# Kernel optimization log

Hardware: AMD Instinct MI355X
Metric: run time of the kernel (lower is better)

The kernel has to match this reference:

```python
import jax, jax.numpy as jnp
import numpy as np

BITS_I, BITS_W = 8, 8
GROUP = 36
DIR_I = (0, 1, 2, 3)
DIR_W = (0, 1, 2, 3)


def bfp_quantize(x, bits, group_size, perm):
    """Block floating point: groups of `group_size` elements (after permuting
    axes by `perm` and flattening) share one exponent (exponent of max abs);
    mantissas are rounded to `bits` signed bits."""
    inv_perm = tuple(np.argsort(perm))
    xp = jnp.transpose(x, perm)
    shape = xp.shape
    flat = xp.reshape(-1)
    n = flat.shape[0]
    pad = (-n) % group_size
    flat = jnp.pad(flat, (0, pad))
    g = flat.reshape(-1, group_size)
    maxabs = jnp.max(jnp.abs(g), axis=1, keepdims=True)
    e = jnp.floor(jnp.log2(jnp.maximum(maxabs, jnp.float32(1e-38))))
    scale = jnp.exp2(e - (bits - 1))  # shared group exponent, `bits` mantissa bits
    qmax = 2 ** (bits - 1) - 1
    q = jnp.clip(jnp.round(g / scale), -qmax - 1, qmax) * scale
    q = jnp.where(maxabs == 0, jnp.float32(0), q)
    out = q.reshape(-1)[:n].reshape(shape)
    return jnp.transpose(out, inv_perm)


def conv2d(x, w, b, stride=1, padding=1, dilation=1, groups=1):
    out = jax.lax.conv_general_dilated(
        x, w,
        window_strides=(stride, stride),
        padding=[(padding, padding), (padding, padding)],
        rhs_dilation=(dilation, dilation),
        feature_group_count=groups,
        dimension_numbers=('NCHW', 'OIHW', 'NCHW'))
    if b is not None:
        out = out + b[None, :, None, None]
    return out


def setup_inputs() -> dict:
    key = jax.random.key(0)
    k1, k2, k3 = jax.random.split(key, 3)
    x = jax.random.normal(k1, (16, 256, 56, 56), dtype=jnp.float32)
    fan_in = 256 * 3 * 3
    bound = 1.0 / np.sqrt(fan_in)
    weight = jax.random.uniform(k2, (256, 256, 3, 3), dtype=jnp.float32,
                                minval=-np.sqrt(6.0 / fan_in), maxval=np.sqrt(6.0 / fan_in))
    bias = jax.random.uniform(k3, (256,), dtype=jnp.float32, minval=-bound, maxval=bound)
    return {"x": x, "weight": weight, "bias": bias}


def reference(x, weight, bias):
    xq = bfp_quantize(x, BITS_I, GROUP, DIR_I)
    wq = bfp_quantize(weight, BITS_W, GROUP, DIR_W)
    return conv2d(xq, wq, bias, stride=1, padding=1, dilation=1, groups=1)
```

## Files before the change

kernel.cpp:

```cpp
#include <hip/hip_runtime.h>

typedef short short8 __attribute__((ext_vector_type(8)));
typedef float f32x4 __attribute__((ext_vector_type(4)));
typedef unsigned short u16;
typedef __attribute__((address_space(3))) unsigned lds_u32_t;
typedef __attribute__((address_space(1))) const unsigned glb_u32_t;

namespace {
constexpr int NIMG = 16;
constexpr int CIN  = 256;
constexpr int HIMG = 56;
constexpr int WIMG = 56;
constexpr int KOUT = 256;
constexpr int PIX  = HIMG * WIMG;
constexpr int HPAD = 58;
constexpr int PP   = HPAD * HPAD;
constexpr int TILES = 26;
constexpr int NX   = NIMG * CIN * PIX;
constexpr int NWEL = KOUT * CIN * 9;
constexpr int XQ_HALVES = NIMG * 32 * PP * 8;
constexpr int CHUNK = 8 * PIX;
constexpr int XBLK = NIMG * 32;
constexpr int WB   = 64;
constexpr int NWG  = NIMG * TILES * 4;
constexpr int CPX  = NWG / 8;
}

__global__ __launch_bounds__(256) void quant_fused(
        const float* __restrict__ x, u16* __restrict__ xq2,
        const float* __restrict__ wsrc, u16* __restrict__ wt3) {
    __shared__ u16 ot[CHUNK];
    const int b = blockIdx.x;
    const int t = threadIdx.x;

    if (b < XBLK) {
        const long s  = (long)b * CHUNK;
        const int  g0 = (int)(s / 36);
        const int  g1 = (int)((s + CHUNK - 1) / 36);

        if (t < 228) {
            int ph, pw;
            if (t < 58)       { ph = 0;  pw = t; }
            else if (t < 116) { ph = 57; pw = t - 58; }
            else { int r = t - 116; ph = 1 + (r >> 1); pw = (r & 1) * 57; }
            *(uint4*)(xq2 + ((size_t)b * PP + ph * HPAD + pw) * 8) =
                make_uint4(0, 0, 0, 0);
        }

        for (int g = g0 + t; g <= g1; g += 256) {
            const long e0 = (long)g * 36;
            float v[36];
            if (e0 + 36 <= (long)NX) {
                const float4* p4 = (const float4*)(x + e0);
#pragma unroll
                for (int j = 0; j < 9; j++) {
                    float4 q4 = p4[j];
                    v[4*j+0] = q4.x; v[4*j+1] = q4.y;
                    v[4*j+2] = q4.z; v[4*j+3] = q4.w;
                }
            } else {
                for (int j = 0; j < 36; j++)
                    v[j] = (e0 + j < (long)NX) ? x[e0 + j] : 0.f;
            }
            float ma = 0.f;
#pragma unroll
            for (int j = 0; j < 36; j++) ma = fmaxf(ma, fabsf(v[j]));
            float scale = 0.f, rinv = 0.f;
            if (ma != 0.f) {
                float e = floorf(log2f(ma));
                scale = exp2f(e - 7.f);
                rinv  = exp2f(7.f - e);
            }
            const long o = e0 - s;
#pragma unroll
            for (int j = 0; j < 36; j += 2) {
                float qa = fminf(fmaxf(rintf(v[j]   * rinv), -128.f), 127.f) * scale;
                float qb = fminf(fmaxf(rintf(v[j+1] * rinv), -128.f), 127.f) * scale;
                uint pk = (__float_as_uint(qa) >> 16)
                        | ((__float_as_uint(qb) >> 16) << 16);
                long oo = o + j;
                if (oo >= 0 && oo < CHUNK)
                    *(uint*)&ot[oo] = pk;
            }
        }
        __syncthreads();

        for (int p = t; p < PIX; p += 256) {
            short8 o8;
#pragma unroll
            for (int cl = 0; cl < 8; cl++)
                o8[cl] = (short)ot[cl * PIX + p];
            int ph = p / WIMG + 1, pw = p % WIMG + 1;
            *(short8*)(xq2 + ((size_t)b * PP + ph * HPAD + pw) * 8) = o8;
        }
    } else {
        int g = (b - XBLK) * 256 + t;
        int base = g * 36;
        float v[36];
        const float4* p4 = (const float4*)(wsrc + base);
#pragma unroll
        for (int j = 0; j < 9; j++) {
            float4 tt = p4[j];
            v[4*j+0] = tt.x; v[4*j+1] = tt.y; v[4*j+2] = tt.z; v[4*j+3] = tt.w;
        }
        float ma = 0.f;
#pragma unroll
        for (int j = 0; j < 36; j++) ma = fmaxf(ma, fabsf(v[j]));
        float scale = 0.f, rinv = 0.f;
        if (ma != 0.f) {
            float e = floorf(log2f(ma));
            scale = exp2f(e - 7.f);
            rinv  = exp2f(7.f - e);
        }
        int k  = g >> 6;
        int c0 = (g & 63) * 4;
#pragma unroll
        for (int j = 0; j < 36; j++) {
            float q = rintf(v[j] * rinv);
            q = fminf(fmaxf(q, -128.f), 127.f) * scale;
            int c  = c0 + j / 9;
            int rs = j % 9;
            int idx = ((((rs * 4 + (c >> 6)) * 8 + ((c >> 3) & 7)) * KOUT) + k) * 8 + (c & 7);
            wt3[idx] = (u16)(__float_as_uint(q) >> 16);
        }
    }
}

#define LOADA(dst_, c_)                                                        \
    {                                                                          \
        const int csp_ = (c_) / 18;                                            \
        const int rsk_ = ((c_) % 18) / 2;                                      \
        const int sub_ = (c_) & 1;                                             \
        const u16* ap_ = wt3 + (rsk_ * 4 + csp_) * 16384 + sub_ * 8192;        \
        _Pragma("unroll")                                                      \
        for (int i_ = 0; i_ < 4; i_++)                                         \
            dst_[i_] = *(const short8*)(ap_ + aOff + i_ * 128);                \
    }

__global__ __launch_bounds__(256, 4) void conv_kernel(
        const u16* __restrict__ xq2, const u16* __restrict__ wt3,
        const float* __restrict__ bias, float* __restrict__ out) {
    __shared__ u16 lB[16384];

    const int tid  = threadIdx.x;
    const int lane = tid & 63;
    const int wv   = tid >> 6;

    const int work = ((int)blockIdx.x & 7) * CPX + ((int)blockIdx.x >> 3);
    const int kq   = work & 3;
    const int pair = work >> 2;
    const int n    = pair / TILES;
    const int t0   = (pair % TILES) * 128;

    const int frow = lane & 15;
    const int fkk  = lane >> 4;
    const int aOff = fkk * 2048 + (kq * 64 + frow) * 8;
    const int bcol = wv * 32 + frow;

    f32x4 acc[4][2] = {};
    short8 a0[4], a1[4], a2[4];

    LOADA(a0, 0);
    LOADA(a1, 1);
    LOADA(a2, 2);

#pragma unroll
    for (int s = 0; s < 4; s++) {
        __syncthreads();
#pragma unroll
        for (int l = 0; l < 8; l++) {
            const int oct = wv * 2 + (l >> 2);
            const int q   = l & 3;
            __builtin_amdgcn_global_load_lds(
                (glb_u32_t*)(xq2 + ((size_t)(n * 32 + s * 8 + oct) * PP
                                    + t0 + q * 64 + lane) * 8),
                (lds_u32_t*)(lB + oct * 2048 + q * 512 + lane * 8),
                16, 0, 0);
        }
        __syncthreads();

#pragma unroll
        for (int k = 0; k < 18; k++) {
            const int c   = 18 * s + k;
            const int rs  = k >> 1;
            const int sub = k & 1;
            const int doff = (rs / 3) * HPAD + (rs % 3);

            short8 bf[2];
#pragma unroll
            for (int j = 0; j < 2; j++)
                bf[j] = *(const short8*)(lB + (sub * 4 + fkk) * 2048
                                         + (doff + bcol + j * 16) * 8);

            __builtin_amdgcn_s_setprio(1);
#pragma unroll
            for (int i = 0; i < 4; i++)
#pragma unroll
                for (int j = 0; j < 2; j++)
                    acc[i][j] = __builtin_amdgcn_mfma_f32_16x16x32_bf16(
                        (k % 3 == 0) ? a0[i] : (k % 3 == 1) ? a1[i] : a2[i],
                        bf[j], acc[i][j], 0, 0, 0);
            __builtin_amdgcn_s_setprio(0);

            if (c + 3 < 72) {
                if (k % 3 == 0)      LOADA(a0, c + 3)
                else if (k % 3 == 1) LOADA(a1, c + 3)
                else                 LOADA(a2, c + 3)
            }
        }
    }

    const int kbase = kq * 64 + fkk * 4;
    const int mbase = wv * 32 + frow;
#pragma unroll
    for (int j = 0; j < 2; j++) {
        int ppp = t0 + mbase + j * 16;
        int h = ppp / HPAD, w = ppp % HPAD;
        if (w < WIMG && h < HIMG) {
            float* ob = out + (size_t)n * KOUT * PIX + h * WIMG + w;
#pragma unroll
            for (int i = 0; i < 4; i++) {
                int kch = kbase + i * 16;
#pragma unroll
                for (int r = 0; r < 4; r++)
                    ob[(size_t)(kch + r) * PIX] = acc[i][j][r] + bias[kch + r];
            }
        }
    }
}

extern "C" void kernel_launch(void* const* d_in, const int* in_sizes, int n_in,
                              void* d_out, int out_size, void* d_ws, size_t ws_size,
                              hipStream_t stream) {
    const float* x   = (const float*)d_in[0];
    const float* wgt = (const float*)d_in[1];
    const float* bs  = (const float*)d_in[2];
    float* out = (float*)d_out;

    u16* xq2 = (u16*)d_ws;
    u16* wt3 = xq2 + XQ_HALVES;

    quant_fused<<<XBLK + WB, 256, 0, stream>>>(x, xq2, wgt, wt3);
    conv_kernel<<<NWG, 256, 0, stream>>>(xq2, wt3, bs, out);
}
```

Baseline: 173.5 us.

## Switch conv to 32x32x16 MFMA with 128x128 output tiles per workgroup

The conv kernel now uses 32x32x16 bf16 MFMA instead of 16x16x32. Each workgroup computes 128 output channels by 128 pixels, arranged as a 2x2 wave grid, so the number of workgroups is halved. Each LDS-staged input tile is therefore reused across twice as many output channels, which cuts global loads and LDS traffic per FLOP. The cost is larger per-wave register tiles and fewer workgroups, which lowers parallelism and makes the weight-register pipeline deeper (144 steps).

Result: faster. 168.2 us (-3.1%).

```diff
diff --git a/kernel.cpp b/kernel.cpp
--- a/kernel.cpp
+++ b/kernel.cpp
@@ -1,7 +1,7 @@
 #include <hip/hip_runtime.h>
 
 typedef short short8 __attribute__((ext_vector_type(8)));
-typedef float f32x4 __attribute__((ext_vector_type(4)));
+typedef float f32x16 __attribute__((ext_vector_type(16)));
 typedef unsigned short u16;
 typedef __attribute__((address_space(3))) unsigned lds_u32_t;
 typedef __attribute__((address_space(1))) const unsigned glb_u32_t;
@@ -22,7 +22,7 @@
 constexpr int CHUNK = 8 * PIX;
 constexpr int XBLK = NIMG * 32;
 constexpr int WB   = 64;
-constexpr int NWG  = NIMG * TILES * 4;
+constexpr int NWG  = NIMG * TILES * 2;
 constexpr int CPX  = NWG / 8;
 }
 
@@ -128,13 +128,14 @@
 
 #define LOADA(dst_, c_)                                                        \
     {                                                                          \
-        const int csp_ = (c_) / 18;                                            \
-        const int rsk_ = ((c_) % 18) / 2;                                      \
-        const int sub_ = (c_) & 1;                                             \
-        const u16* ap_ = wt3 + (rsk_ * 4 + csp_) * 16384 + sub_ * 8192;        \
+        const int csp_ = (c_) / 36;                                            \
+        const int m_   = (c_) % 36;                                            \
+        const int rs_  = m_ >> 2;                                              \
+        const int sk_  = m_ & 3;                                               \
+        const u16* ap_ = wt3 + (rs_ * 4 + csp_) * 16384 + sk_ * 4096;          \
         _Pragma("unroll")                                                      \
-        for (int i_ = 0; i_ < 4; i_++)                                         \
-            dst_[i_] = *(const short8*)(ap_ + aOff + i_ * 128);                \
+        for (int i_ = 0; i_ < 2; i_++)                                         \
+            dst_[i_] = *(const short8*)(ap_ + aOff + i_ * 256);                \
     }
 
 __global__ __launch_bounds__(256, 4) void conv_kernel(
@@ -147,18 +148,18 @@
     const int wv   = tid >> 6;
 
     const int work = ((int)blockIdx.x & 7) * CPX + ((int)blockIdx.x >> 3);
-    const int kq   = work & 3;
-    const int pair = work >> 2;
+    const int k0   = (work & 1) * 128;
+    const int pair = work >> 1;
     const int n    = pair / TILES;
     const int t0   = (pair % TILES) * 128;
 
-    const int frow = lane & 15;
-    const int fkk  = lane >> 4;
-    const int aOff = fkk * 2048 + (kq * 64 + frow) * 8;
-    const int bcol = wv * 32 + frow;
-
-    f32x4 acc[4][2] = {};
-    short8 a0[4], a1[4], a2[4];
+    const int lrow = lane & 31;
+    const int lhk  = lane >> 5;
+    const int aOff = lhk * 2048 + (k0 + (wv >> 1) * 64 + lrow) * 8;
+    const int bOff = lhk * 2048 + ((wv & 1) * 64 + lrow) * 8;
+
+    f32x16 acc[2][2] = {};
+    short8 a0[2], a1[2], a2[2];
 
     LOADA(a0, 0);
     LOADA(a1, 1);
@@ -180,51 +181,51 @@
         __syncthreads();
 
 #pragma unroll
-        for (int k = 0; k < 18; k++) {
-            const int c   = 18 * s + k;
-            const int rs  = k >> 1;
-            const int sub = k & 1;
+        for (int m = 0; m < 36; m++) {
+            const int c   = 36 * s + m;
+            const int rs  = m >> 2;
+            const int sk  = m & 3;
             const int doff = (rs / 3) * HPAD + (rs % 3);
 
             short8 bf[2];
 #pragma unroll
             for (int j = 0; j < 2; j++)
-                bf[j] = *(const short8*)(lB + (sub * 4 + fkk) * 2048
-                                         + (doff + bcol + j * 16) * 8);
+                bf[j] = *(const short8*)(lB + sk * 4096 + bOff
+                                         + (doff + j * 32) * 8);
 
             __builtin_amdgcn_s_setprio(1);
 #pragma unroll
-            for (int i = 0; i < 4; i++)
+            for (int i = 0; i < 2; i++)
 #pragma unroll
                 for (int j = 0; j < 2; j++)
-                    acc[i][j] = __builtin_amdgcn_mfma_f32_16x16x32_bf16(
-                        (k % 3 == 0) ? a0[i] : (k % 3 == 1) ? a1[i] : a2[i],
+                    acc[i][j] = __builtin_amdgcn_mfma_f32_32x32x16_bf16(
+                        (m % 3 == 0) ? a0[i] : (m % 3 == 1) ? a1[i] : a2[i],
                         bf[j], acc[i][j], 0, 0, 0);
             __builtin_amdgcn_s_setprio(0);
 
-            if (c + 3 < 72) {
-                if (k % 3 == 0)      LOADA(a0, c + 3)
-                else if (k % 3 == 1) LOADA(a1, c + 3)
+            if (c + 3 < 144) {
+                if (m % 3 == 0)      LOADA(a0, c + 3)
+                else if (m % 3 == 1) LOADA(a1, c + 3)
                 else                 LOADA(a2, c + 3)
             }
         }
     }
 
-    const int kbase = kq * 64 + fkk * 4;
-    const int mbase = wv * 32 + frow;
+    const int kw   = k0 + (wv >> 1) * 64 + 4 * lhk;
+    const int colb = t0 + (wv & 1) * 64 + lrow;
 #pragma unroll
     for (int j = 0; j < 2; j++) {
-        int ppp = t0 + mbase + j * 16;
+        int ppp = colb + j * 32;
         int h = ppp / HPAD, w = ppp % HPAD;
         if (w < WIMG && h < HIMG) {
             float* ob = out + (size_t)n * KOUT * PIX + h * WIMG + w;
 #pragma unroll
-            for (int i = 0; i < 4; i++) {
-                int kch = kbase + i * 16;
-#pragma unroll
-                for (int r = 0; r < 4; r++)
-                    ob[(size_t)(kch + r) * PIX] = acc[i][j][r] + bias[kch + r];
-            }
+            for (int i = 0; i < 2; i++)
+#pragma unroll
+                for (int r = 0; r < 16; r++) {
+                    int kr = kw + i * 32 + (r & 3) + 8 * (r >> 2);
+                    ob[(size_t)kr * PIX] = acc[i][j][r] + bias[kr];
+                }
         }
     }
 }
```
